# Optimization experiments

Hardware: AMD Instinct MI355X
Metric: run time of the kernel (lower is better)

## Reference

```python
import jax, jax.numpy as jnp
import numpy as np

N, M, D = 8192, 8192, 512

def setup_inputs() -> dict:
    key = jax.random.key(0)
    ks = jax.random.split(key, 8)
    s = 1.0 / np.sqrt(D)
    return {
        "x": jax.random.normal(ks[0], (N, D), jnp.float32),
        "domain_x": jax.random.normal(ks[1], (M, D), jnp.float32),
        "Wq": jax.random.normal(ks[2], (D, D), jnp.float32) * s,
        "bq": jax.random.normal(ks[3], (D,), jnp.float32) * s,
        "Wk": jax.random.normal(ks[4], (D, D), jnp.float32) * s,
        "bk": jax.random.normal(ks[5], (D,), jnp.float32) * s,
        "Wv": jax.random.normal(ks[6], (D, D), jnp.float32) * s,
        "bv": jax.random.normal(ks[7], (D,), jnp.float32) * s,
    }

def reference(x, domain_x, Wq, bq, Wk, bk, Wv, bv):
    # torch Linear: y = x @ W^T + b
    q = x @ Wq.T + bq            # [N, D]
    k = domain_x @ Wk.T + bk     # [M, D]
    v = domain_x @ Wv.T + bv     # [M, D]
    scale = jnp.sqrt(jnp.asarray(k.shape[-1], q.dtype))
    scores = q @ k.T             # [N, M]
    attn = jax.nn.softmax(scores / scale, axis=-1)
    return attn @ v              # [N, D]
```

## Files before the change

### kernel.cpp

```cpp
#include <hip/hip_runtime.h>
#include <stdint.h>


#define DEV __device__ __forceinline__

typedef short short8 __attribute__((ext_vector_type(8)));
typedef float floatx4 __attribute__((ext_vector_type(4)));
typedef unsigned int uintx4 __attribute__((ext_vector_type(4)));
typedef unsigned short ushortx4 __attribute__((ext_vector_type(4)));

constexpr int NN = 8192;
constexpr int MM = 8192;
constexpr int DD = 512;
constexpr float SCALE2 = 0.0637587160f;

#define NEG_INF (-__builtin_inff())

#if defined(__has_builtin)
#if __has_builtin(__builtin_amdgcn_exp2f)
#define EXP2F(x) __builtin_amdgcn_exp2f(x)
#else
#define EXP2F(x) exp2f(x)
#endif
#else
#define EXP2F(x) exp2f(x)
#endif

DEV unsigned short f2bf(float f) {
  unsigned u = __builtin_bit_cast(unsigned, f);
  return (unsigned short)((u + 0x7FFFu + ((u >> 16) & 1u)) >> 16);
}
DEV float bf2f(unsigned short h) {
  unsigned u = ((unsigned)h) << 16;
  return __builtin_bit_cast(float, u);
}

DEV short8 ld_s8(const void* p) {
  short8 v; __builtin_memcpy(&v, __builtin_assume_aligned(p, 16), 16); return v;
}
DEV uintx4 ld_u4(const void* p) {
  uintx4 v; __builtin_memcpy(&v, __builtin_assume_aligned(p, 16), 16); return v;
}
DEV void st_u4(void* p, uintx4 v) {
  __builtin_memcpy(__builtin_assume_aligned(p, 16), &v, 16);
}
DEV void st_us4(void* p, ushortx4 v) {
  __builtin_memcpy(__builtin_assume_aligned(p, 8), &v, 8);
}
DEV float4 ld_f4(const void* p) {
  float4 v; __builtin_memcpy(&v, __builtin_assume_aligned(p, 16), 16); return v;
}

DEV void async_lds16(const void* g, const void* l) {
  __builtin_amdgcn_global_load_lds(
      (const __attribute__((address_space(1))) unsigned int*)g,
      (__attribute__((address_space(3))) unsigned int*)l, 16, 0, 0);
}

__global__ void prep_w(const float* __restrict__ Wq, const float* __restrict__ Wk,
                       const float* __restrict__ Wv, unsigned short* __restrict__ Wb) {
  const int z = blockIdx.z;
  const float* src = (z == 0) ? Wq : (z == 1) ? Wk : Wv;
  unsigned short* dst = Wb + (size_t)z * DD * DD;
  size_t idx = ((size_t)blockIdx.x * 256 + threadIdx.x) * 8;
  float4 a = ld_f4(src + idx);
  float4 b = ld_f4(src + idx + 4);
  ushortx4 lo = {f2bf(a.x), f2bf(a.y), f2bf(a.z), f2bf(a.w)};
  ushortx4 hi = {f2bf(b.x), f2bf(b.y), f2bf(b.z), f2bf(b.w)};
  st_us4(dst + idx, lo);
  st_us4(dst + idx + 4, hi);
}

__global__ __launch_bounds__(256, 2)
void qkv_proj(const float* __restrict__ x, const float* __restrict__ dx,
              const unsigned short* __restrict__ Wb,
              const float* __restrict__ bq, const float* __restrict__ bk,
              const float* __restrict__ bv,
              unsigned short* __restrict__ Qb, unsigned short* __restrict__ Kb,
              unsigned short* __restrict__ VTb) {
  const int z = blockIdx.z;
  const float* A = (z == 0) ? x : dx;
  const unsigned short* W = Wb + (size_t)z * DD * DD;
  const float* bias = (z == 0) ? bq : (z == 1) ? bk : bv;

  const int r0 = blockIdx.x * 64;
  const int c0 = blockIdx.y * 256;
  const int tid = threadIdx.x;
  const int lane = tid & 63;
  const int wave = tid >> 6;
  const int lr = lane & 15;
  const int quad = lane >> 4;

  __shared__ __align__(16) unsigned short As[64 * 64];
  __shared__ __align__(16) unsigned short Ws[256 * 64];

  floatx4 o[16];
#pragma unroll
  for (int i = 0; i < 16; ++i) o[i] = {0.f, 0.f, 0.f, 0.f};

  for (int k0 = 0; k0 < DD; k0 += 64) {
#pragma unroll
    for (int i = 0; i < 4; ++i) {
      int idx = i * 256 + tid;
      int r = idx >> 4, c4 = idx & 15;
      float4 v = ld_f4(A + (size_t)(r0 + r) * DD + k0 + c4 * 4);
      ushortx4 pk = {f2bf(v.x), f2bf(v.y), f2bf(v.z), f2bf(v.w)};
      st_us4(&As[r * 64 + (((c4 >> 1) ^ (r & 7)) * 8) + (c4 & 1) * 4], pk);
    }
#pragma unroll
    for (int i = 0; i < 8; ++i) {
      int idx = i * 256 + tid;
      int r = idx >> 3, c = idx & 7;
      uintx4 v = ld_u4(W + (size_t)(c0 + r) * DD + k0 + c * 8);
      st_u4(&Ws[r * 64 + ((c ^ (r & 7)) * 8)], v);
    }
    __syncthreads();

    short8 a[2];
#pragma unroll
    for (int ks = 0; ks < 2; ++ks)
      a[ks] = ld_s8(&As[(wave * 16 + lr) * 64 + (((ks * 4 + quad) ^ (lr & 7)) * 8)]);
#pragma unroll
    for (int ct = 0; ct < 16; ++ct) {
#pragma unroll
      for (int ks = 0; ks < 2; ++ks) {
        short8 b = ld_s8(&Ws[(ct * 16 + lr) * 64 + (((ks * 4 + quad) ^ (lr & 7)) * 8)]);
        o[ct] = __builtin_amdgcn_mfma_f32_16x16x32_bf16(a[ks], b, o[ct], 0, 0, 0);
      }
    }
    __syncthreads();
  }

#pragma unroll
  for (int ct = 0; ct < 16; ++ct) {
    int col = c0 + ct * 16 + lr;
    float bv_ = bias[col];
    int rowb = r0 + wave * 16 + quad * 4;
    if (z == 2) {
      ushortx4 pk = {f2bf(o[ct][0] + bv_), f2bf(o[ct][1] + bv_),
                     f2bf(o[ct][2] + bv_), f2bf(o[ct][3] + bv_)};
      st_us4(VTb + (size_t)col * MM + rowb, pk);
    } else {
      unsigned short* Outp = (z == 0) ? Qb : Kb;
      float sc = (z == 0) ? SCALE2 : 1.f;
#pragma unroll
      for (int r = 0; r < 4; ++r)
        Outp[(size_t)(rowb + r) * DD + col] = f2bf((o[ct][r] + bv_) * sc);
    }
  }
}

template <int SPLITS_, int LOG2S_>
__global__ __launch_bounds__(256, 2)
void flash_attn(const unsigned short* __restrict__ Qb,
                const unsigned short* __restrict__ Kb,
                const unsigned short* __restrict__ VTb,
                unsigned short* __restrict__ Opart,
                float* __restrict__ Mpart, float* __restrict__ Lpart) {
  constexpr int MT = MM / SPLITS_;
  constexpr int ITERS = MT / 64;
  const int lin = blockIdx.x;
  const int split = lin & (SPLITS_ - 1);
  const int n0 = (lin >> LOG2S_) * 64;
  const int m_begin = split * MT;

  const int tid = threadIdx.x;
  const int lane = tid & 63;
  const int wave = tid >> 6;
  const int lr = lane & 15;
  const int quad = lane >> 4;

  __shared__ __align__(16) unsigned short sKV[33280];
  __shared__ __align__(16) unsigned short sP[64 * 76];
  __shared__ float sAlpha[64];

  short8 qf[16];
  {
    const unsigned short* qptr = Qb + (size_t)(n0 + wave * 16 + lr) * DD + quad * 8;
#pragma unroll
    for (int ks = 0; ks < 16; ++ks) qf[ks] = ld_s8(qptr + ks * 32);
  }

  const int vrb = lane >> 3;
  const int vcb = ((lane & 7) ^ vrb) * 8;
  const unsigned short* vsrc0 = VTb + (size_t)(wave * 128 + vrb) * MM + vcb;
  unsigned short* vdst0 = &sKV[wave * 16 * 512];

  floatx4 o[32];
#pragma unroll
  for (int i = 0; i < 32; ++i) o[i] = {0.f, 0.f, 0.f, 0.f};
  float mrow[4] = {NEG_INF, NEG_INF, NEG_INF, NEG_INF};
  float lrow[4] = {0.f, 0.f, 0.f, 0.f};

  for (int it = 0; it < ITERS; ++it) {
    const int m0 = m_begin + it * 64;

#pragma unroll
    for (int i = 0; i < 16; ++i) {
      const int r = wave * 16 + i;
      async_lds16(Kb + (size_t)(m0 + r) * DD + lane * 8, &sKV[r * 520]);
    }
    __syncthreads();

    floatx4 s[4];
#pragma unroll
    for (int ct = 0; ct < 4; ++ct) s[ct] = {0.f, 0.f, 0.f, 0.f};
#pragma unroll
    for (int ks = 0; ks < 16; ++ks) {
      const unsigned short* kb = &sKV[ks * 32 + quad * 8];
#pragma unroll
      for (int ct = 0; ct < 4; ++ct) {
        short8 b = ld_s8(kb + (ct * 16 + lr) * 520);
        s[ct] = __builtin_amdgcn_mfma_f32_16x16x32_bf16(qf[ks], b, s[ct], 0, 0, 0);
      }
    }
    __syncthreads();

    {
      const unsigned short* src = vsrc0 + m0;
#pragma unroll
      for (int j = 0; j < 16; ++j)
        async_lds16(src + (size_t)j * 8 * MM, vdst0 + j * 512);
    }

    float alpha[4];
#pragma unroll
    for (int r = 0; r < 4; ++r) {
      float mx = fmaxf(fmaxf(s[0][r], s[1][r]), fmaxf(s[2][r], s[3][r]));
      mx = fmaxf(mx, __shfl_xor(mx, 1));
      mx = fmaxf(mx, __shfl_xor(mx, 2));
      mx = fmaxf(mx, __shfl_xor(mx, 4));
      mx = fmaxf(mx, __shfl_xor(mx, 8));
      float mnew = fmaxf(mrow[r], mx);
      alpha[r] = EXP2F(mrow[r] - mnew);
      mrow[r] = mnew;
      float rs = 0.f;
#pragma unroll
      for (int ct = 0; ct < 4; ++ct) {
        float p = EXP2F(s[ct][r] - mnew);
        s[ct][r] = p;
        rs += p;
      }
      rs += __shfl_xor(rs, 1);
      rs += __shfl_xor(rs, 2);
      rs += __shfl_xor(rs, 4);
      rs += __shfl_xor(rs, 8);
      lrow[r] = lrow[r] * alpha[r] + rs;
    }
    if (lr == 0) {
#pragma unroll
      for (int r = 0; r < 4; ++r) sAlpha[wave * 16 + quad * 4 + r] = alpha[r];
    }

#pragma unroll
    for (int ct = 0; ct < 4; ++ct)
#pragma unroll
      for (int r = 0; r < 4; ++r)
        sP[(wave * 16 + quad * 4 + r) * 76 + ct * 16 + lr] = f2bf(s[ct][r]);

    __syncthreads();

    floatx4 af[4];
#pragma unroll
    for (int rt = 0; rt < 4; ++rt) {
      float4 t = ld_f4(&sAlpha[rt * 16 + quad * 4]);
      af[rt] = {t.x, t.y, t.z, t.w};
    }
    bool need = false;
#pragma unroll
    for (int rt = 0; rt < 4; ++rt)
#pragma unroll
      for (int r = 0; r < 4; ++r) need = need || (af[rt][r] < 1.f);
    if (__any(need)) {
#pragma unroll
      for (int rt = 0; rt < 4; ++rt)
#pragma unroll
        for (int ct = 0; ct < 8; ++ct)
#pragma unroll
          for (int r = 0; r < 4; ++r) o[rt * 8 + ct][r] *= af[rt][r];
    }

#pragma unroll
    for (int ks = 0; ks < 2; ++ks) {
      short8 pa[4];
#pragma unroll
      for (int rt = 0; rt < 4; ++rt)
        pa[rt] = ld_s8(&sP[(rt * 16 + lr) * 76 + ks * 32 + quad * 8]);
#pragma unroll
      for (int ct = 0; ct < 8; ++ct) {
        const int r = wave * 128 + ct * 16 + lr;
        short8 b = ld_s8(&sKV[r * 64 + (((ks * 4 + quad) ^ (lr & 7)) * 8)]);
#pragma unroll
        for (int rt = 0; rt < 4; ++rt)
          o[rt * 8 + ct] = __builtin_amdgcn_mfma_f32_16x16x32_bf16(pa[rt], b,
                                                                   o[rt * 8 + ct], 0, 0, 0);
      }
    }
    __syncthreads();
  }

  unsigned short* op = Opart + (size_t)split * NN * DD;
#pragma unroll
  for (int rt = 0; rt < 4; ++rt)
#pragma unroll
    for (int ct = 0; ct < 8; ++ct) {
      int row = n0 + rt * 16 + quad * 4;
      int col = wave * 128 + ct * 16 + lr;
#pragma unroll
      for (int r = 0; r < 4; ++r)
        op[(size_t)(row + r) * DD + col] = f2bf(o[rt * 8 + ct][r]);
    }
  const int grow = n0 + wave * 16 + quad * 4;
  if (lr == 0) {
#pragma unroll
    for (int r = 0; r < 4; ++r) {
      Mpart[split * NN + grow + r] = mrow[r];
      Lpart[split * NN + grow + r] = lrow[r];
    }
  }
}

template <int SPLITS_>
__global__ void combine_kernel(const unsigned short* __restrict__ Op,
                               const float* __restrict__ Mp,
                               const float* __restrict__ Lp,
                               float* __restrict__ out) {
  constexpr size_t NDv = (size_t)NN * DD;
  size_t base = ((size_t)blockIdx.x * 256 + threadIdx.x) * 8;
  int n = (int)(base >> 9);
  float mv[SPLITS_];
  float ms = NEG_INF;
#pragma unroll
  for (int s = 0; s < SPLITS_; ++s) {
    mv[s] = Mp[s * NN + n];
    ms = fmaxf(ms, mv[s]);
  }
  float num[8];
#pragma unroll
  for (int j = 0; j < 8; ++j) num[j] = 0.f;
  float den = 0.f;
#pragma unroll
  for (int s = 0; s < SPLITS_; ++s) {
    float w = EXP2F(mv[s] - ms);
    den += w * Lp[s * NN + n];
    uintx4 u = ld_u4(Op + s * NDv + base);
#pragma unroll
    for (int j = 0; j < 4; ++j) {
      num[2 * j]     += w * bf2f((unsigned short)(u[j] & 0xffffu));
      num[2 * j + 1] += w * bf2f((unsigned short)(u[j] >> 16));
    }
  }
  float inv = 1.f / den;
  float4 o0 = {num[0] * inv, num[1] * inv, num[2] * inv, num[3] * inv};
  float4 o1 = {num[4] * inv, num[5] * inv, num[6] * inv, num[7] * inv};
  __builtin_memcpy(__builtin_assume_aligned(out + base, 16), &o0, 16);
  __builtin_memcpy(__builtin_assume_aligned(out + base + 4, 16), &o1, 16);
}

extern "C" void kernel_launch(void* const* d_in, const int* in_sizes, int n_in,
                              void* d_out, int out_size, void* d_ws, size_t ws_size,
                              hipStream_t stream) {
  const float* x  = (const float*)d_in[0];
  const float* dx = (const float*)d_in[1];
  const float* Wq = (const float*)d_in[2];
  const float* bq = (const float*)d_in[3];
  const float* Wk = (const float*)d_in[4];
  const float* bk = (const float*)d_in[5];
  const float* Wv = (const float*)d_in[6];
  const float* bv = (const float*)d_in[7];
  float* out = (float*)d_out;

  const size_t ND = (size_t)NN * DD;
  const size_t WBE = (size_t)3 * DD * DD;
  unsigned short* Qb  = (unsigned short*)d_ws;
  unsigned short* Kb  = Qb + ND;
  unsigned short* VTb = Kb + ND;
  unsigned short* Wb  = VTb + ND;
  unsigned short* Op  = Wb + WBE;

  auto bytes_for = [&](size_t S) {
    return (3 * ND + WBE + S * ND) * 2 + S * (size_t)NN * 8;
  };
  const int splits = (ws_size >= bytes_for(4)) ? 4 : 2;
  float* Mp = (float*)(Op + (size_t)splits * ND);
  float* Lp = Mp + (size_t)splits * NN;

  hipLaunchKernelGGL(prep_w, dim3(DD * DD / 2048, 1, 3), dim3(256), 0, stream,
                     Wq, Wk, Wv, Wb);
  hipLaunchKernelGGL(qkv_proj, dim3(NN / 64, 2, 3), dim3(256), 0, stream,
                     x, dx, Wb, bq, bk, bv, Qb, Kb, VTb);
  if (splits == 4) {
    hipLaunchKernelGGL((flash_attn<4, 2>), dim3(NN / 64 * 4), dim3(256), 0, stream,
                       Qb, Kb, VTb, Op, Mp, Lp);
    hipLaunchKernelGGL(combine_kernel<4>, dim3((unsigned)(ND / 2048)), dim3(256), 0, stream,
                       Op, Mp, Lp, out);
  } else {
    hipLaunchKernelGGL((flash_attn<2, 1>), dim3(NN / 64 * 2), dim3(256), 0, stream,
                       Qb, Kb, VTb, Op, Mp, Lp);
    hipLaunchKernelGGL(combine_kernel<2>, dim3((unsigned)(ND / 2048)), dim3(256), 0, stream,
                       Op, Mp, Lp, out);
  }
}
```

Measured before the change: 347.8 us.

## Double flash-attention query tile to 128 rows with 8 waves per block

```diff
diff --git a/kernel.cpp b/kernel.cpp
--- a/kernel.cpp
+++ b/kernel.cpp
@@ -151,7 +151,7 @@
 }
 
 template <int SPLITS_, int LOG2S_>
-__global__ __launch_bounds__(256, 2)
+__global__ __launch_bounds__(512, 2)
 void flash_attn(const unsigned short* __restrict__ Qb,
                 const unsigned short* __restrict__ Kb,
                 const unsigned short* __restrict__ VTb,
@@ -161,7 +161,7 @@
   constexpr int ITERS = MT / 64;
   const int lin = blockIdx.x;
   const int split = lin & (SPLITS_ - 1);
-  const int n0 = (lin >> LOG2S_) * 64;
+  const int n0 = (lin >> LOG2S_) * 128;
   const int m_begin = split * MT;
 
   const int tid = threadIdx.x;
@@ -170,9 +170,10 @@
   const int lr = lane & 15;
   const int quad = lane >> 4;
 
-  __shared__ __align__(16) unsigned short sKV[33280];
-  __shared__ __align__(16) unsigned short sP[64 * 76];
-  __shared__ float sAlpha[64];
+  __shared__ __align__(16) unsigned short sK[64 * 520];
+  __shared__ __align__(16) unsigned short sP[128 * 76];
+  __shared__ __align__(16) float sAlpha[128];
+  __shared__ int sFlag[8];
 
   short8 qf[16];
   {
@@ -183,8 +184,8 @@
 
   const int vrb = lane >> 3;
   const int vcb = ((lane & 7) ^ vrb) * 8;
-  const unsigned short* vsrc0 = VTb + (size_t)(wave * 128 + vrb) * MM + vcb;
-  unsigned short* vdst0 = &sKV[wave * 16 * 512];
+  const unsigned short* vsrc0 = VTb + (size_t)(wave * 64 + vrb) * MM + vcb;
+  unsigned short* vdst0 = &sK[wave * 8 * 512];
 
   floatx4 o[32];
 #pragma unroll
@@ -196,9 +197,9 @@
     const int m0 = m_begin + it * 64;
 
 #pragma unroll
-    for (int i = 0; i < 16; ++i) {
-      const int r = wave * 16 + i;
-      async_lds16(Kb + (size_t)(m0 + r) * DD + lane * 8, &sKV[r * 520]);
+    for (int i = 0; i < 8; ++i) {
+      const int r = wave * 8 + i;
+      async_lds16(Kb + (size_t)(m0 + r) * DD + lane * 8, &sK[r * 520]);
     }
     __syncthreads();
 
@@ -207,7 +208,7 @@
     for (int ct = 0; ct < 4; ++ct) s[ct] = {0.f, 0.f, 0.f, 0.f};
 #pragma unroll
     for (int ks = 0; ks < 16; ++ks) {
-      const unsigned short* kb = &sKV[ks * 32 + quad * 8];
+      const unsigned short* kb = &sK[ks * 32 + quad * 8];
 #pragma unroll
       for (int ct = 0; ct < 4; ++ct) {
         short8 b = ld_s8(kb + (ct * 16 + lr) * 520);
@@ -219,7 +220,7 @@
     {
       const unsigned short* src = vsrc0 + m0;
 #pragma unroll
-      for (int j = 0; j < 16; ++j)
+      for (int j = 0; j < 8; ++j)
         async_lds16(src + (size_t)j * 8 * MM, vdst0 + j * 512);
     }
 
@@ -247,9 +248,14 @@
       rs += __shfl_xor(rs, 8);
       lrow[r] = lrow[r] * alpha[r] + rs;
     }
-    if (lr == 0) {
-#pragma unroll
-      for (int r = 0; r < 4; ++r) sAlpha[wave * 16 + quad * 4 + r] = alpha[r];
+    {
+      bool nd = (alpha[0] < 1.f) || (alpha[1] < 1.f) || (alpha[2] < 1.f) || (alpha[3] < 1.f);
+      int any = __any(nd) ? 1 : 0;
+      if (lane == 0) sFlag[wave] = any;
+      if (lr == 0) {
+#pragma unroll
+        for (int r = 0; r < 4; ++r) sAlpha[wave * 16 + quad * 4 + r] = alpha[r];
+      }
     }
 
 #pragma unroll
@@ -260,40 +266,37 @@
 
     __syncthreads();
 
-    floatx4 af[4];
-#pragma unroll
-    for (int rt = 0; rt < 4; ++rt) {
-      float4 t = ld_f4(&sAlpha[rt * 16 + quad * 4]);
-      af[rt] = {t.x, t.y, t.z, t.w};
-    }
-    bool need = false;
-#pragma unroll
-    for (int rt = 0; rt < 4; ++rt)
-#pragma unroll
-      for (int r = 0; r < 4; ++r) need = need || (af[rt][r] < 1.f);
-    if (__any(need)) {
-#pragma unroll
-      for (int rt = 0; rt < 4; ++rt)
-#pragma unroll
-        for (int ct = 0; ct < 8; ++ct)
-#pragma unroll
-          for (int r = 0; r < 4; ++r) o[rt * 8 + ct][r] *= af[rt][r];
+#pragma unroll
+    for (int rt = 0; rt < 8; ++rt) {
+      if (sFlag[rt]) {
+        float4 t = ld_f4(&sAlpha[rt * 16 + quad * 4]);
+#pragma unroll
+        for (int ct = 0; ct < 4; ++ct) {
+          o[rt * 4 + ct][0] *= t.x;
+          o[rt * 4 + ct][1] *= t.y;
+          o[rt * 4 + ct][2] *= t.z;
+          o[rt * 4 + ct][3] *= t.w;
+        }
+      }
     }
 
 #pragma unroll
     for (int ks = 0; ks < 2; ++ks) {
-      short8 pa[4];
-#pragma unroll
-      for (int rt = 0; rt < 4; ++rt)
-        pa[rt] = ld_s8(&sP[(rt * 16 + lr) * 76 + ks * 32 + quad * 8]);
-#pragma unroll
-      for (int ct = 0; ct < 8; ++ct) {
-        const int r = wave * 128 + ct * 16 + lr;
-        short8 b = ld_s8(&sKV[r * 64 + (((ks * 4 + quad) ^ (lr & 7)) * 8)]);
-#pragma unroll
-        for (int rt = 0; rt < 4; ++rt)
-          o[rt * 8 + ct] = __builtin_amdgcn_mfma_f32_16x16x32_bf16(pa[rt], b,
-                                                                   o[rt * 8 + ct], 0, 0, 0);
+#pragma unroll
+      for (int rth = 0; rth < 2; ++rth) {
+        short8 pa[4];
+#pragma unroll
+        for (int i = 0; i < 4; ++i)
+          pa[i] = ld_s8(&sP[((rth * 4 + i) * 16 + lr) * 76 + ks * 32 + quad * 8]);
+#pragma unroll
+        for (int ct = 0; ct < 4; ++ct) {
+          const int r = wave * 64 + ct * 16 + lr;
+          short8 b = ld_s8(&sK[r * 64 + (((ks * 4 + quad) ^ (lr & 7)) * 8)]);
+#pragma unroll
+          for (int i = 0; i < 4; ++i)
+            o[(rth * 4 + i) * 4 + ct] = __builtin_amdgcn_mfma_f32_16x16x32_bf16(
+                pa[i], b, o[(rth * 4 + i) * 4 + ct], 0, 0, 0);
+        }
       }
     }
     __syncthreads();
@@ -301,14 +304,14 @@
 
   unsigned short* op = Opart + (size_t)split * NN * DD;
 #pragma unroll
-  for (int rt = 0; rt < 4; ++rt)
-#pragma unroll
-    for (int ct = 0; ct < 8; ++ct) {
+  for (int rt = 0; rt < 8; ++rt)
+#pragma unroll
+    for (int ct = 0; ct < 4; ++ct) {
       int row = n0 + rt * 16 + quad * 4;
-      int col = wave * 128 + ct * 16 + lr;
+      int col = wave * 64 + ct * 16 + lr;
 #pragma unroll
       for (int r = 0; r < 4; ++r)
-        op[(size_t)(row + r) * DD + col] = f2bf(o[rt * 8 + ct][r]);
+        op[(size_t)(row + r) * DD + col] = f2bf(o[rt * 4 + ct][r]);
     }
   const int grow = n0 + wave * 16 + quad * 4;
   if (lr == 0) {
@@ -390,12 +393,12 @@
   hipLaunchKernelGGL(qkv_proj, dim3(NN / 64, 2, 3), dim3(256), 0, stream,
                      x, dx, Wb, bq, bk, bv, Qb, Kb, VTb);
   if (splits == 4) {
-    hipLaunchKernelGGL((flash_attn<4, 2>), dim3(NN / 64 * 4), dim3(256), 0, stream,
+    hipLaunchKernelGGL((flash_attn<4, 2>), dim3(NN / 128 * 4), dim3(512), 0, stream,
                        Qb, Kb, VTb, Op, Mp, Lp);
     hipLaunchKernelGGL(combine_kernel<4>, dim3((unsigned)(ND / 2048)), dim3(256), 0, stream,
                        Op, Mp, Lp, out);
   } else {
-    hipLaunchKernelGGL((flash_attn<2, 1>), dim3(NN / 64 * 2), dim3(256), 0, stream,
+    hipLaunchKernelGGL((flash_attn<2, 1>), dim3(NN / 128 * 2), dim3(512), 0, stream,
                        Qb, Kb, VTb, Op, Mp, Lp);
     hipLaunchKernelGGL(combine_kernel<2>, dim3((unsigned)(ND / 2048)), dim3(256), 0, stream,
                        Op, Mp, Lp, out);
```

Result: no change. 351.2 us (+1.0%).
